# Kernel optimization log

Measured on AMD Instinct MI355X. Metric: run time of the kernel, lower is better.

## Reference

```python
import jax, jax.numpy as jnp
import numpy as np

B, S, D, K = 8, 2048, 512, 64

def setup_inputs() -> dict:
    key = jax.random.key(0)
    k1, k2, k3 = jax.random.split(key, 3)
    # glorot_uniform for weights, zeros for biases (matching Keras build)
    lim = float(np.sqrt(6.0 / (D + K)))
    return {
        "inputs": jax.random.normal(k1, (B, S, D), dtype=jnp.float32),
        "key_extract": jax.random.uniform(k2, (D, K), dtype=jnp.float32, minval=-lim, maxval=lim),
        "key_bias": jnp.zeros((1, K), dtype=jnp.float32),
        "query_extract": jax.random.uniform(k3, (D, K), dtype=jnp.float32, minval=-lim, maxval=lim),
        "query_bias": jnp.zeros((1, K), dtype=jnp.float32),
    }

def reference(inputs, key_extract, key_bias, query_extract, query_bias):
    # keys/query: [B, S, K]
    keys = jnp.einsum("bsd,dk->bsk", inputs, key_extract) + key_bias
    query = jnp.einsum("bsd,dk->bsk", inputs, query_extract) + query_bias
    # logits: [B, S, S] = query @ keys^T (no 1/sqrt(K) scaling in original)
    logits = jnp.einsum("bqk,bsk->bqs", query, keys)
    # NON-STANDARD: softmax over axis=1 (the query axis), not the last axis
    attn = jax.nn.softmax(logits, axis=1)
    # weighted_input: [B, S, D], raw inputs used as V
    return jnp.einsum("bqs,bsd->bqd", attn, inputs)
```

## Files before the change

### kernel.cpp

```cpp
#include <hip/hip_runtime.h>
#include <hip/hip_bf16.h>

#define Bn 8
#define Sn 2048
#define Dn 512
#define Kn 64

typedef _Float16 half8 __attribute__((ext_vector_type(8)));
typedef _Float16 half4v __attribute__((ext_vector_type(4)));
typedef float f32x4 __attribute__((ext_vector_type(4)));

#define MFMA16(a,b,c) __builtin_amdgcn_mfma_f32_16x16x32_f16(a,b,c,0,0,0)
#define LOG2E 1.4426950408889634f

__device__ __forceinline__ half8 ldfrag(const _Float16* base, int row, int k8){
    const int scol = k8 ^ (row & 7);
    return *(const half8*)((const char*)base + row*128 + scol*16);
}


__global__ __launch_bounds__(256) void wtrans_kernel(
    const float* __restrict__ Wk, const float* __restrict__ Wq,
    _Float16* __restrict__ Wt16)
{
    const int n = blockIdx.x;
    const int t = threadIdx.x;
    const float* src = (n < 64) ? Wq : Wk;
    const int nn = n & 63;
    #pragma unroll
    for (int i = 0; i < 2; ++i){
        const int k = t + 256*i;
        Wt16[(size_t)n*Dn + k] = (_Float16)src[(size_t)k*Kn + nn];
    }
}

__global__ __launch_bounds__(256, 2) void prep_kernel(
    const float* __restrict__ X, const _Float16* __restrict__ Wt16,
    const float* __restrict__ bk, const float* __restrict__ bq,
    _Float16* __restrict__ Qh2, _Float16* __restrict__ Kh2,
    _Float16* __restrict__ Vt2)
{
    __shared__ _Float16 Xt[2][32*64];
    const int bid = blockIdx.x;
    const int b = bid & 7, sb32 = bid >> 3;
    const int tid = threadIdx.x, lane = tid & 63, w = tid >> 6;
    const int l15 = lane & 15, l4 = lane >> 4;

    const int srow = tid >> 3, sg = tid & 7;
    const float* Xs = X + ((size_t)(b*Sn + sb32*32) + srow)*Dn + sg*8;
    const int sdst = srow*128 + (((sg ^ (srow & 7) ^ (srow >> 3)) & 7) * 16);

    const int n0 = w*32 + l15;
    const _Float16* Wp0 = Wt16 + (size_t)n0*Dn + l4*8;
    const _Float16* Wp1 = Wp0 + (size_t)16*Dn;

    f32x4 acc[2][2];
    #pragma unroll
    for (int i = 0; i < 2; ++i)
        #pragma unroll
        for (int j = 0; j < 2; ++j){ f32x4 z = {0.f,0.f,0.f,0.f}; acc[i][j] = z; }

    {
        const float4 v0 = *(const float4*)(Xs);
        const float4 v1 = *(const float4*)(Xs + 4);
        half8 h;
        h[0]=(_Float16)v0.x; h[1]=(_Float16)v0.y; h[2]=(_Float16)v0.z; h[3]=(_Float16)v0.w;
        h[4]=(_Float16)v1.x; h[5]=(_Float16)v1.y; h[6]=(_Float16)v1.z; h[7]=(_Float16)v1.w;
        *(half8*)((char*)Xt[0] + sdst) = h;
    }
    __syncthreads();

    const int dcol = w*16 + l15;
    #pragma unroll
    for (int kc = 0; kc < 8; ++kc){
        const _Float16* XtC = Xt[kc & 1];
        float4 nv0, nv1;
        if (kc < 7){
            nv0 = *(const float4*)(Xs + (kc+1)*64);
            nv1 = *(const float4*)(Xs + (kc+1)*64 + 4);
        }
        const half8 wf00 = *(const half8*)(Wp0 + kc*64);
        const half8 wf01 = *(const half8*)(Wp0 + kc*64 + 32);
        const half8 wf10 = *(const half8*)(Wp1 + kc*64);
        const half8 wf11 = *(const half8*)(Wp1 + kc*64 + 32);
        #pragma unroll
        for (int ks = 0; ks < 2; ++ks){
            #pragma unroll
            for (int qt = 0; qt < 2; ++qt){
                const int rw = qt*16 + l15;
                const int g = ((ks*4 + l4) ^ (rw & 7) ^ (rw >> 3)) & 7;
                const half8 a = *(const half8*)((const char*)XtC + rw*128 + g*16);
                acc[qt][0] = MFMA16(a, ks ? wf01 : wf00, acc[qt][0]);
                acc[qt][1] = MFMA16(a, ks ? wf11 : wf10, acc[qt][1]);
            }
        }
        {
            half8 hv;
            #pragma unroll
            for (int e = 0; e < 8; ++e){
                const int rw = l4*8 + e;
                const int g = ((dcol >> 3) ^ e ^ l4) & 7;
                hv[e] = XtC[rw*64 + g*8 + (dcol & 7)];
            }
            const size_t G = (((size_t)(b*32 + (sb32 >> 1))*2 + (sb32 & 1))*32 + kc*4 + w)*64 + lane;
            *(half8*)(Vt2 + G*8) = hv;
        }
        if (kc < 7){
            half8 h;
            h[0]=(_Float16)nv0.x; h[1]=(_Float16)nv0.y; h[2]=(_Float16)nv0.z; h[3]=(_Float16)nv0.w;
            h[4]=(_Float16)nv1.x; h[5]=(_Float16)nv1.y; h[6]=(_Float16)nv1.z; h[7]=(_Float16)nv1.w;
            *(half8*)((char*)Xt[(kc+1) & 1] + sdst) = h;
        }
        __syncthreads();
    }

    _Float16* tile16 = &Xt[0][0];
    #pragma unroll
    for (int qt = 0; qt < 2; ++qt){
        const int ql = qt*16 + l4*4;
        #pragma unroll
        for (int nt = 0; nt < 2; ++nt){
            const int n = w*32 + nt*16 + l15;
            const bool isQ = (n < 64);
            const float bias = isQ ? bq[n] : bk[n - 64];
            const float scale = isQ ? LOG2E : 1.0f;
            #pragma unroll
            for (int r = 0; r < 4; ++r)
                tile16[(ql + r)*128 + n] = (_Float16)((acc[qt][nt][r] + bias) * scale);
        }
    }
    __syncthreads();
    #pragma unroll
    for (int i = 0; i < 2; ++i){
        const int g = tid + 256*i;
        const int isK = g >> 8, qtl = (g >> 7) & 1, ks = (g >> 6) & 1, ln = g & 63;
        const int l4g = ln >> 4, l15g = ln & 15;
        const half8 h = *(const half8*)&tile16[(qtl*16 + l15g)*128 + isK*64 + ks*32 + l4g*8];
        const size_t tg = (size_t)b*128 + sb32*2 + qtl;
        _Float16* dst = (isK ? Kh2 : Qh2) + ((tg*2 + ks)*64 + ln)*8;
        *(half8*)dst = h;
    }
}

#define SBODY(QC0,QC1,QC2,QC3, QN0,QN1,QN2,QN3) do { \
    QN0 = *(const half8*)(Qp); \
    QN1 = *(const half8*)(Qp + 1024); \
    QN2 = *(const half8*)(Qp + 2048); \
    QN3 = *(const half8*)(Qp + 3072); \
    Qp += 8192; \
    f32x4 c0 = cinit, c1 = cinit; \
    c0 = MFMA16(ka0, QC0, c0); c0 = MFMA16(ka1, QC1, c0); \
    c1 = MFMA16(ka0, QC2, c1); c1 = MFMA16(ka1, QC3, c1); \
    _Pragma("unroll") \
    for (int r = 0; r < 4; ++r) \
        z[r] += exp2f(c0[r]) + exp2f(c1[r]); \
} while(0)

__global__ __launch_bounds__(512, 2) void stats_kernel(
    const _Float16* __restrict__ Qh2, const _Float16* __restrict__ Kh2,
    float* __restrict__ CS)
{
    __shared__ float zred[2][64];
    const int bid = blockIdx.x;
    const int b = bid & 7, stb = bid >> 3;
    const int tid = threadIdx.x, lane = tid & 63, w = tid >> 6;
    const int l15 = lane & 15, l4 = lane >> 4;
    const int sw = w & 3, qh = w >> 2, qh2 = qh*2;

    const half8 ka0 = *(const half8*)(Kh2 + ((size_t)((b*128 + stb*4 + sw)*2 + 0)*64 + lane)*8);
    const half8 ka1 = *(const half8*)(Kh2 + ((size_t)((b*128 + stb*4 + sw)*2 + 1)*64 + lane)*8);

    const char* Qp = (const char*)Qh2 + (size_t)(b*128 + qh2)*2048 + lane*16;

    const f32x4 cinit = {-64.f, -64.f, -64.f, -64.f};
    float z[4] = {0.f, 0.f, 0.f, 0.f};

    half8 qbA0, qbA1, qbA2, qbA3, qbB0, qbB1, qbB2, qbB3;
    qbA0 = *(const half8*)(Qp);
    qbA1 = *(const half8*)(Qp + 1024);
    qbA2 = *(const half8*)(Qp + 2048);
    qbA3 = *(const half8*)(Qp + 3072);
    Qp += 8192;

    for (int qc = 0; qc < 32; qc += 2){
        SBODY(qbA0,qbA1,qbA2,qbA3, qbB0,qbB1,qbB2,qbB3);
        SBODY(qbB0,qbB1,qbB2,qbB3, qbA0,qbA1,qbA2,qbA3);
    }
    #pragma unroll
    for (int d = 1; d < 16; d <<= 1)
        #pragma unroll
        for (int r = 0; r < 4; ++r)
            z[r] += __shfl_xor(z[r], d);
    if (l15 == 0){
        const int sl = sw*16 + l4*4;
        #pragma unroll
        for (int r = 0; r < 4; ++r) zred[qh][sl+r] = z[r];
    }
    __syncthreads();
    if (tid < 64)
        CS[b*Sn + stb*64 + tid] = -(64.0f + __log2f(zred[0][tid] + zred[1][tid]));
}

#define WRP(PT, QT, C) do { \
    half4v p; \
    p[0] = (_Float16)exp2f(C[0]); \
    p[1] = (_Float16)exp2f(C[1]); \
    p[2] = (_Float16)exp2f(C[2]); \
    p[3] = (_Float16)exp2f(C[3]); \
    const int q_ = (QT)*16 + l15; \
    *(half4v*)((char*)(PT) + q_*128 + (sb2 ^ ((q_ & 7) << 4))) = p; \
} while(0)

#define ABODY(KA, KAN, VB, VBN, CSV, CSN, PT) do { \
    f32x4 c0 = {CSV.x, CSV.y, CSV.z, CSV.w}; \
    f32x4 c1 = c0, c2 = c0, c3 = c0; \
    c0 = MFMA16(KA[0], qb[0][0], c0); c0 = MFMA16(KA[1], qb[0][1], c0); \
    c1 = MFMA16(KA[0], qb[1][0], c1); c1 = MFMA16(KA[1], qb[1][1], c1); \
    c2 = MFMA16(KA[0], qb[2][0], c2); c2 = MFMA16(KA[1], qb[2][1], c2); \
    c3 = MFMA16(KA[0], qb[3][0], c3); c3 = MFMA16(KA[1], qb[3][1], c3); \
    KAN[0] = *(const half8*)(Kp); \
    KAN[1] = *(const half8*)(Kp + 1024); \
    Kp += 8192; \
    WRP(PT, 0, c0); WRP(PT, 1, c1); \
    WRP(PT, 2, c2); WRP(PT, 3, c3); \
    asm volatile("s_waitcnt lgkmcnt(0)\n\ts_barrier" ::: "memory"); \
    CSN = *(const float4*)Cp; Cp += 64; \
    _Pragma("unroll") \
    for (int d_ = 0; d_ < 4; ++d_){ \
        VBN[d_]   = *(const half8*)(Vp0 + d_*1024); \
        VBN[4+d_] = *(const half8*)(Vp1 + d_*1024); \
    } \
    Vp0 += 65536; Vp1 += 65536; \
    __builtin_amdgcn_s_setprio(1); \
    _Pragma("unroll") \
    for (int ks = 0; ks < 2; ++ks){ \
        const half8 pa0 = ldfrag(PT, 0*16 + l15, ks*4 + l4); \
        const half8 pa1 = ldfrag(PT, 1*16 + l15, ks*4 + l4); \
        const half8 pa2 = ldfrag(PT, 2*16 + l15, ks*4 + l4); \
        const half8 pa3 = ldfrag(PT, 3*16 + l15, ks*4 + l4); \
        _Pragma("unroll") \
        for (int d_ = 0; d_ < 4; ++d_){ \
            acc[0][d_] = MFMA16(pa0, VB[ks*4+d_], acc[0][d_]); \
            acc[1][d_] = MFMA16(pa1, VB[ks*4+d_], acc[1][d_]); \
            acc[2][d_] = MFMA16(pa2, VB[ks*4+d_], acc[2][d_]); \
            acc[3][d_] = MFMA16(pa3, VB[ks*4+d_], acc[3][d_]); \
        } \
    } \
    __builtin_amdgcn_s_setprio(0); \
} while(0)

__global__ __launch_bounds__(256, 2) void attn_kernel(
    const _Float16* __restrict__ Qh2, const _Float16* __restrict__ Kh2,
    const _Float16* __restrict__ Vt2, const float* __restrict__ CS,
    float* __restrict__ out)
{
    __shared__ _Float16 Pt[2][64*64];
    const int bid = blockIdx.x;
    const int b  = bid & 7;
    const int qi = (bid >> 3) & 31;
    const int dh = bid >> 8;
    const int q0 = qi * 64;
    const int tid = threadIdx.x, lane = tid & 63, w = tid >> 6;
    const int l15 = lane & 15, l4 = lane >> 4;
    const int soff = w*16 + l4*4;
    const int sb2  = soff * 2;

    const size_t qgb = (size_t)b*128 + qi*4;
    half8 qb[4][2];
    #pragma unroll
    for (int qt = 0; qt < 4; ++qt)
        #pragma unroll
        for (int ks = 0; ks < 2; ++ks)
            qb[qt][ks] = *(const half8*)(Qh2 + (((qgb + qt)*2 + ks)*64 + lane)*8);

    const char* Kp  = (const char*)Kh2 + (size_t)(b*128 + w)*2048 + lane*16;
    const char* Vp0 = (const char*)Vt2 + (size_t)(b*2048 + dh*16 + w*4)*1024 + lane*16;
    const char* Vp1 = Vp0 + 32768;
    const float* Cp = CS + b*Sn + soff;

    half8 kaA[2], kaB[2], vbA[8], vbB[8];
    float4 csA, csB;
    kaA[0] = *(const half8*)(Kp);
    kaA[1] = *(const half8*)(Kp + 1024);
    Kp += 8192;
    #pragma unroll
    for (int d_ = 0; d_ < 4; ++d_){
        vbA[d_]   = *(const half8*)(Vp0 + d_*1024);
        vbA[4+d_] = *(const half8*)(Vp1 + d_*1024);
    }
    Vp0 += 65536; Vp1 += 65536;
    csA = *(const float4*)Cp; Cp += 64;

    f32x4 acc[4][4];
    #pragma unroll
    for (int i = 0; i < 4; ++i)
        #pragma unroll
        for (int j = 0; j < 4; ++j){ f32x4 zz4 = {0.f,0.f,0.f,0.f}; acc[i][j] = zz4; }

    for (int it = 0; it < 16; ++it){
        ABODY(kaA, kaB, vbA, vbB, csA, csB, Pt[0]);
        ABODY(kaB, kaA, vbB, vbA, csB, csA, Pt[1]);
    }

    float* ob = out + (size_t)(b*Sn + q0)*Dn + dh*256 + w*64;
    #pragma unroll
    for (int qt = 0; qt < 4; ++qt){
        const int q = qt*16 + l4*4;
        #pragma unroll
        for (int d_ = 0; d_ < 4; ++d_){
            #pragma unroll
            for (int r = 0; r < 4; ++r)
                ob[(size_t)(q + r)*Dn + d_*16 + l15] = acc[qt][d_][r];
        }
    }
}

extern "C" void kernel_launch(void* const* d_in, const int* in_sizes, int n_in,
                              void* d_out, int out_size, void* d_ws, size_t ws_size,
                              hipStream_t stream)
{
    const float* X  = (const float*)d_in[0];
    const float* Wk = (const float*)d_in[1];
    const float* bk = (const float*)d_in[2];
    const float* Wq = (const float*)d_in[3];
    const float* bq = (const float*)d_in[4];
    float* out = (float*)d_out;

    char* ws = (char*)d_ws;
    _Float16* Qh2  = (_Float16*)ws;
    _Float16* Kh2  = (_Float16*)(ws + ((size_t)2 << 20));
    _Float16* Vt2  = (_Float16*)(ws + ((size_t)4 << 20));
    float*    CS   = (float*)(ws + ((size_t)20 << 20));
    _Float16* Wt16 = (_Float16*)(ws + ((size_t)20 << 20) + (2 << 16));

    wtrans_kernel<<<dim3(128), dim3(256), 0, stream>>>(Wk, Wq, Wt16);
    prep_kernel<<<dim3(Bn*(Sn/32)), dim3(256), 0, stream>>>(X, Wt16, bk, bq, Qh2, Kh2, Vt2);
    stats_kernel<<<dim3(Bn*(Sn/64)), dim3(512), 0, stream>>>(Qh2, Kh2, CS);
    attn_kernel<<<dim3(Bn*(Sn/64)*2), dim3(256), 0, stream>>>(Qh2, Kh2, Vt2, CS, out);
}
```

Before: 82.29 us.

## Double query tile per block and stage V tiles in LDS via direct global-to-LDS loads

The attention kernel now uses 512-thread blocks covering 128 queries instead of 64, halving the grid. Each V tile is loaded once per block into shared memory with global_load_lds and double-buffered, so eight waves share it rather than each wave holding V in registers. Shared-memory offsets are precomputed, and an extra barrier per step protects the buffers. This cuts global V traffic and register pressure, but adds LDS reads, barrier synchronisation and a larger shared-memory footprint that may lower occupancy.

```diff
diff --git a/kernel.cpp b/kernel.cpp
--- a/kernel.cpp
+++ b/kernel.cpp
@@ -12,6 +12,12 @@
 
 #define MFMA16(a,b,c) __builtin_amdgcn_mfma_f32_16x16x32_f16(a,b,c,0,0,0)
 #define LOG2E 1.4426950408889634f
+
+__device__ __forceinline__ void glds16(const void* g, void* l){
+    __builtin_amdgcn_global_load_lds(
+        (const __attribute__((address_space(1))) unsigned int*)g,
+        (__attribute__((address_space(3))) unsigned int*)l, 16, 0, 0);
+}
 
 __device__ __forceinline__ half8 ldfrag(const _Float16* base, int row, int k8){
     const int scol = k8 ^ (row & 7);
@@ -201,18 +207,21 @@
         CS[b*Sn + stb*64 + tid] = -(64.0f + __log2f(zred[0][tid] + zred[1][tid]));
 }
 
-#define WRP(PT, QT, C) do { \
+#define WRP(CUR, QT, C) do { \
     half4v p; \
     p[0] = (_Float16)exp2f(C[0]); \
     p[1] = (_Float16)exp2f(C[1]); \
     p[2] = (_Float16)exp2f(C[2]); \
     p[3] = (_Float16)exp2f(C[3]); \
-    const int q_ = (QT)*16 + l15; \
-    *(half4v*)((char*)(PT) + q_*128 + (sb2 ^ ((q_ & 7) << 4))) = p; \
+    *(half4v*)((char*)Pt[CUR] + pwo[QT]) = p; \
 } while(0)
 
-#define ABODY(KA, KAN, VB, VBN, CSV, CSN, PT) do { \
-    f32x4 c0 = {CSV.x, CSV.y, CSV.z, CSV.w}; \
+#define ABODY(CUR, KA, KAN, CSA, CSN, SCV) do { \
+    { const size_t sb_ = Vbase + (size_t)((SCV)+1)*65536; \
+      _Pragma("unroll") \
+      for (int j = 0; j < 4; ++j) \
+        glds16(Vt2c + sb_ + soff[j], (char*)VL[(CUR)^1] + (w*4+j)*1024); } \
+    f32x4 c0 = {CSA.x, CSA.y, CSA.z, CSA.w}; \
     f32x4 c1 = c0, c2 = c0, c3 = c0; \
     c0 = MFMA16(KA[0], qb[0][0], c0); c0 = MFMA16(KA[1], qb[0][1], c0); \
     c1 = MFMA16(KA[0], qb[1][0], c1); c1 = MFMA16(KA[1], qb[1][1], c1); \
@@ -221,51 +230,46 @@
     KAN[0] = *(const half8*)(Kp); \
     KAN[1] = *(const half8*)(Kp + 1024); \
     Kp += 8192; \
-    WRP(PT, 0, c0); WRP(PT, 1, c1); \
-    WRP(PT, 2, c2); WRP(PT, 3, c3); \
-    asm volatile("s_waitcnt lgkmcnt(0)\n\ts_barrier" ::: "memory"); \
     CSN = *(const float4*)Cp; Cp += 64; \
-    _Pragma("unroll") \
-    for (int d_ = 0; d_ < 4; ++d_){ \
-        VBN[d_]   = *(const half8*)(Vp0 + d_*1024); \
-        VBN[4+d_] = *(const half8*)(Vp1 + d_*1024); \
-    } \
-    Vp0 += 65536; Vp1 += 65536; \
-    __builtin_amdgcn_s_setprio(1); \
-    _Pragma("unroll") \
-    for (int ks = 0; ks < 2; ++ks){ \
-        const half8 pa0 = ldfrag(PT, 0*16 + l15, ks*4 + l4); \
-        const half8 pa1 = ldfrag(PT, 1*16 + l15, ks*4 + l4); \
-        const half8 pa2 = ldfrag(PT, 2*16 + l15, ks*4 + l4); \
-        const half8 pa3 = ldfrag(PT, 3*16 + l15, ks*4 + l4); \
+    WRP(CUR, 0, c0); WRP(CUR, 1, c1); WRP(CUR, 2, c2); WRP(CUR, 3, c3); \
+    asm volatile("s_waitcnt lgkmcnt(0) vmcnt(4)\n\ts_barrier" ::: "memory"); \
+    { const char* PB = (const char*)Pt[CUR]; \
+      const char* VB_ = (const char*)VL[CUR]; \
+      _Pragma("unroll") \
+      for (int ks = 0; ks < 2; ++ks){ \
+        const half8 pa0 = *(const half8*)(PB + pao[0][ks]); \
+        const half8 pa1 = *(const half8*)(PB + pao[1][ks]); \
+        const half8 pa2 = *(const half8*)(PB + pao[2][ks]); \
+        const half8 pa3 = *(const half8*)(PB + pao[3][ks]); \
         _Pragma("unroll") \
-        for (int d_ = 0; d_ < 4; ++d_){ \
-            acc[0][d_] = MFMA16(pa0, VB[ks*4+d_], acc[0][d_]); \
-            acc[1][d_] = MFMA16(pa1, VB[ks*4+d_], acc[1][d_]); \
-            acc[2][d_] = MFMA16(pa2, VB[ks*4+d_], acc[2][d_]); \
-            acc[3][d_] = MFMA16(pa3, VB[ks*4+d_], acc[3][d_]); \
+        for (int dt = 0; dt < 4; ++dt){ \
+            const half8 vb = *(const half8*)(VB_ + vbo[ks][dt]); \
+            acc[0][dt] = MFMA16(pa0, vb, acc[0][dt]); \
+            acc[1][dt] = MFMA16(pa1, vb, acc[1][dt]); \
+            acc[2][dt] = MFMA16(pa2, vb, acc[2][dt]); \
+            acc[3][dt] = MFMA16(pa3, vb, acc[3][dt]); \
         } \
-    } \
-    __builtin_amdgcn_s_setprio(0); \
+      } } \
+    asm volatile("s_barrier" ::: "memory"); \
 } while(0)
 
-__global__ __launch_bounds__(256, 2) void attn_kernel(
+__global__ __launch_bounds__(512, 2) void attn_kernel(
     const _Float16* __restrict__ Qh2, const _Float16* __restrict__ Kh2,
     const _Float16* __restrict__ Vt2, const float* __restrict__ CS,
     float* __restrict__ out)
 {
-    __shared__ _Float16 Pt[2][64*64];
+    __shared__ _Float16 Pt[2][128*64];
+    __shared__ _Float16 VL[2][32*512];
     const int bid = blockIdx.x;
     const int b  = bid & 7;
-    const int qi = (bid >> 3) & 31;
-    const int dh = bid >> 8;
-    const int q0 = qi * 64;
+    const int qi = (bid >> 3) & 15;
+    const int dh = bid >> 7;
+    const int q0 = qi * 128;
     const int tid = threadIdx.x, lane = tid & 63, w = tid >> 6;
     const int l15 = lane & 15, l4 = lane >> 4;
-    const int soff = w*16 + l4*4;
-    const int sb2  = soff * 2;
-
-    const size_t qgb = (size_t)b*128 + qi*4;
+    const int st = w & 3, qh = w >> 2, dw = w & 3;
+
+    const size_t qgb = (size_t)b*128 + qi*8 + qh*4;
     half8 qb[4][2];
     #pragma unroll
     for (int qt = 0; qt < 4; ++qt)
@@ -273,23 +277,44 @@
         for (int ks = 0; ks < 2; ++ks)
             qb[qt][ks] = *(const half8*)(Qh2 + (((qgb + qt)*2 + ks)*64 + lane)*8);
 
-    const char* Kp  = (const char*)Kh2 + (size_t)(b*128 + w)*2048 + lane*16;
-    const char* Vp0 = (const char*)Vt2 + (size_t)(b*2048 + dh*16 + w*4)*1024 + lane*16;
-    const char* Vp1 = Vp0 + 32768;
-    const float* Cp = CS + b*Sn + soff;
-
-    half8 kaA[2], kaB[2], vbA[8], vbB[8];
+    int pwo[4], pao[4][2], vbo[2][4];
+    {
+        const int sb2 = (st*16 + l4*4) * 2;
+        #pragma unroll
+        for (int qt = 0; qt < 4; ++qt){
+            const int q_ = qh*64 + qt*16 + l15;
+            pwo[qt] = q_*128 + (sb2 ^ ((q_ & 7) << 4));
+            #pragma unroll
+            for (int ks = 0; ks < 2; ++ks)
+                pao[qt][ks] = q_*128 + (((ks*4 + l4) ^ (q_ & 7)) * 16);
+        }
+        #pragma unroll
+        for (int ks = 0; ks < 2; ++ks)
+            #pragma unroll
+            for (int dt = 0; dt < 4; ++dt)
+                vbo[ks][dt] = (ks*16 + dw*4 + dt)*1024 + lane*16;
+    }
+    const char* Vt2c = (const char*)Vt2;
+    const size_t Vbase = (size_t)b * (32*65536);
+    size_t soff[4];
+    #pragma unroll
+    for (int j = 0; j < 4; ++j){
+        const int gi = w*4 + j;
+        soff[j] = (size_t)(((gi >> 4)*32) + dh*16 + (gi & 15))*1024 + lane*16;
+    }
+
+    const char* Kp = (const char*)Kh2 + (size_t)(b*128 + st)*2048 + lane*16;
+    const float* Cp = CS + b*Sn + st*16 + l4*4;
+
+    half8 kaA[2], kaB[2];
     float4 csA, csB;
     kaA[0] = *(const half8*)(Kp);
     kaA[1] = *(const half8*)(Kp + 1024);
     Kp += 8192;
-    #pragma unroll
-    for (int d_ = 0; d_ < 4; ++d_){
-        vbA[d_]   = *(const half8*)(Vp0 + d_*1024);
-        vbA[4+d_] = *(const half8*)(Vp1 + d_*1024);
-    }
-    Vp0 += 65536; Vp1 += 65536;
     csA = *(const float4*)Cp; Cp += 64;
+    #pragma unroll
+    for (int j = 0; j < 4; ++j)
+        glds16(Vt2c + Vbase + soff[j], (char*)VL[0] + (w*4+j)*1024);
 
     f32x4 acc[4][4];
     #pragma unroll
@@ -297,20 +322,20 @@
         #pragma unroll
         for (int j = 0; j < 4; ++j){ f32x4 zz4 = {0.f,0.f,0.f,0.f}; acc[i][j] = zz4; }
 
-    for (int it = 0; it < 16; ++it){
-        ABODY(kaA, kaB, vbA, vbB, csA, csB, Pt[0]);
-        ABODY(kaB, kaA, vbB, vbA, csB, csA, Pt[1]);
-    }
-
-    float* ob = out + (size_t)(b*Sn + q0)*Dn + dh*256 + w*64;
+    for (int sc = 0; sc < 32; sc += 2){
+        ABODY(0, kaA, kaB, csA, csB, sc);
+        ABODY(1, kaB, kaA, csB, csA, sc+1);
+    }
+
+    float* ob = out + (size_t)(b*Sn + q0 + qh*64)*Dn + dh*256 + dw*64;
     #pragma unroll
     for (int qt = 0; qt < 4; ++qt){
         const int q = qt*16 + l4*4;
         #pragma unroll
-        for (int d_ = 0; d_ < 4; ++d_){
+        for (int dt = 0; dt < 4; ++dt){
             #pragma unroll
             for (int r = 0; r < 4; ++r)
-                ob[(size_t)(q + r)*Dn + d_*16 + l15] = acc[qt][d_][r];
+                ob[(size_t)(q + r)*Dn + dt*16 + l15] = acc[qt][dt][r];
         }
     }
 }
@@ -336,5 +361,5 @@
     wtrans_kernel<<<dim3(128), dim3(256), 0, stream>>>(Wk, Wq, Wt16);
     prep_kernel<<<dim3(Bn*(Sn/32)), dim3(256), 0, stream>>>(X, Wt16, bk, bq, Qh2, Kh2, Vt2);
     stats_kernel<<<dim3(Bn*(Sn/64)), dim3(512), 0, stream>>>(Qh2, Kh2, CS);
-    attn_kernel<<<dim3(Bn*(Sn/64)*2), dim3(256), 0, stream>>>(Qh2, Kh2, Vt2, CS, out);
-}
+    attn_kernel<<<dim3(Bn*(Sn/128)*2), dim3(512), 0, stream>>>(Qh2, Kh2, Vt2, CS, out);
+}
```

Measured after the change: 89.66 us. +9.0%, slower.

## Materialize unnormalized P in global memory and fold softmax scale into V

Applied to the files above, without the earlier changes.

The stats kernel now computes per-key column max and sum, then runs a second QK^T pass that writes exp(logit - max) as fp16 P tiles to a global buffer. A new vscale kernel multiplies V by the per-key normalization factor. The attention kernel then becomes a pure P·V GEMM streaming P and V from global memory, with no recomputation of QK^T and no LDS exchange or barriers. In exchange it adds a large P write and read (B*S*S fp16, about 64 MB), an extra kernel launch, and precision risk from scaling fp16 V.

```diff
diff --git a/kernel.cpp b/kernel.cpp
--- a/kernel.cpp
+++ b/kernel.cpp
@@ -12,11 +12,6 @@
 
 #define MFMA16(a,b,c) __builtin_amdgcn_mfma_f32_16x16x32_f16(a,b,c,0,0,0)
 #define LOG2E 1.4426950408889634f
-
-__device__ __forceinline__ half8 ldfrag(const _Float16* base, int row, int k8){
-    const int scol = k8 ^ (row & 7);
-    return *(const half8*)((const char*)base + row*128 + scol*16);
-}
 
 
 __global__ __launch_bounds__(256) void wtrans_kernel(
@@ -142,175 +137,210 @@
     }
 }
 
-#define SBODY(QC0,QC1,QC2,QC3, QN0,QN1,QN2,QN3) do { \
-    QN0 = *(const half8*)(Qp); \
-    QN1 = *(const half8*)(Qp + 1024); \
-    QN2 = *(const half8*)(Qp + 2048); \
-    QN3 = *(const half8*)(Qp + 3072); \
-    Qp += 8192; \
-    f32x4 c0 = cinit, c1 = cinit; \
-    c0 = MFMA16(ka0, QC0, c0); c0 = MFMA16(ka1, QC1, c0); \
-    c1 = MFMA16(ka0, QC2, c1); c1 = MFMA16(ka1, QC3, c1); \
-    _Pragma("unroll") \
-    for (int r = 0; r < 4; ++r) \
-        z[r] += exp2f(c0[r]) + exp2f(c1[r]); \
-} while(0)
-
-__global__ __launch_bounds__(512, 2) void stats_kernel(
+__global__ __launch_bounds__(512) void stats2_kernel(
     const _Float16* __restrict__ Qh2, const _Float16* __restrict__ Kh2,
-    float* __restrict__ CS)
-{
-    __shared__ float zred[2][64];
+    _Float16* __restrict__ Pg, float* __restrict__ CSV)
+{
+    __shared__ float mred[8][64];
+    __shared__ float zred[8][64];
+    __shared__ float mfin[64];
+    __shared__ char  tr[8][2048];
     const int bid = blockIdx.x;
     const int b = bid & 7, stb = bid >> 3;
     const int tid = threadIdx.x, lane = tid & 63, w = tid >> 6;
     const int l15 = lane & 15, l4 = lane >> 4;
-    const int sw = w & 3, qh = w >> 2, qh2 = qh*2;
-
-    const half8 ka0 = *(const half8*)(Kh2 + ((size_t)((b*128 + stb*4 + sw)*2 + 0)*64 + lane)*8);
-    const half8 ka1 = *(const half8*)(Kh2 + ((size_t)((b*128 + stb*4 + sw)*2 + 1)*64 + lane)*8);
-
-    const char* Qp = (const char*)Qh2 + (size_t)(b*128 + qh2)*2048 + lane*16;
-
-    const f32x4 cinit = {-64.f, -64.f, -64.f, -64.f};
-    float z[4] = {0.f, 0.f, 0.f, 0.f};
-
-    half8 qbA0, qbA1, qbA2, qbA3, qbB0, qbB1, qbB2, qbB3;
-    qbA0 = *(const half8*)(Qp);
-    qbA1 = *(const half8*)(Qp + 1024);
-    qbA2 = *(const half8*)(Qp + 2048);
-    qbA3 = *(const half8*)(Qp + 3072);
-    Qp += 8192;
-
-    for (int qc = 0; qc < 32; qc += 2){
-        SBODY(qbA0,qbA1,qbA2,qbA3, qbB0,qbB1,qbB2,qbB3);
-        SBODY(qbB0,qbB1,qbB2,qbB3, qbA0,qbA1,qbA2,qbA3);
+
+    half8 ka[4][2];
+    #pragma unroll
+    for (int ssub = 0; ssub < 4; ++ssub)
+        #pragma unroll
+        for (int ks = 0; ks < 2; ++ks)
+            ka[ssub][ks] = *(const half8*)((const char*)Kh2 +
+                (((size_t)(b*128 + stb*4 + ssub)*2 + ks) << 10) + lane*16);
+
+    const char* Qb = (const char*)Qh2 + ((size_t)(b*128 + w*16)*2 << 10) + lane*16;
+
+    f32x4 m4[4], z4[4];
+    #pragma unroll
+    for (int s = 0; s < 4; ++s){
+        f32x4 mi = {-3.0e38f,-3.0e38f,-3.0e38f,-3.0e38f};
+        f32x4 zi = {0.f,0.f,0.f,0.f};
+        m4[s] = mi; z4[s] = zi;
+    }
+    for (int qi = 0; qi < 16; ++qi){
+        const half8 qb0 = *(const half8*)(Qb + qi*2048);
+        const half8 qb1 = *(const half8*)(Qb + qi*2048 + 1024);
+        #pragma unroll
+        for (int ssub = 0; ssub < 4; ++ssub){
+            f32x4 c = {0.f,0.f,0.f,0.f};
+            c = MFMA16(ka[ssub][0], qb0, c);
+            c = MFMA16(ka[ssub][1], qb1, c);
+            #pragma unroll
+            for (int r = 0; r < 4; ++r){
+                m4[ssub][r] = fmaxf(m4[ssub][r], c[r]);
+                z4[ssub][r] += exp2f(c[r] - 64.0f);
+            }
+        }
     }
     #pragma unroll
     for (int d = 1; d < 16; d <<= 1)
         #pragma unroll
-        for (int r = 0; r < 4; ++r)
-            z[r] += __shfl_xor(z[r], d);
+        for (int ssub = 0; ssub < 4; ++ssub)
+            #pragma unroll
+            for (int r = 0; r < 4; ++r){
+                m4[ssub][r] = fmaxf(m4[ssub][r], __shfl_xor(m4[ssub][r], d));
+                z4[ssub][r] += __shfl_xor(z4[ssub][r], d);
+            }
     if (l15 == 0){
-        const int sl = sw*16 + l4*4;
-        #pragma unroll
-        for (int r = 0; r < 4; ++r) zred[qh][sl+r] = z[r];
+        #pragma unroll
+        for (int ssub = 0; ssub < 4; ++ssub)
+            #pragma unroll
+            for (int r = 0; r < 4; ++r){
+                mred[w][ssub*16 + l4*4 + r] = m4[ssub][r];
+                zred[w][ssub*16 + l4*4 + r] = z4[ssub][r];
+            }
     }
     __syncthreads();
-    if (tid < 64)
-        CS[b*Sn + stb*64 + tid] = -(64.0f + __log2f(zred[0][tid] + zred[1][tid]));
-}
-
-#define WRP(PT, QT, C) do { \
-    half4v p; \
-    p[0] = (_Float16)exp2f(C[0]); \
-    p[1] = (_Float16)exp2f(C[1]); \
-    p[2] = (_Float16)exp2f(C[2]); \
-    p[3] = (_Float16)exp2f(C[3]); \
-    const int q_ = (QT)*16 + l15; \
-    *(half4v*)((char*)(PT) + q_*128 + (sb2 ^ ((q_ & 7) << 4))) = p; \
+    if (tid < 64){
+        float M = mred[0][tid], Z = zred[0][tid];
+        #pragma unroll
+        for (int ww = 1; ww < 8; ++ww){
+            M = fmaxf(M, mred[ww][tid]);
+            Z += zred[ww][tid];
+        }
+        mfin[tid] = M;
+        CSV[b*Sn + stb*64 + tid] = exp2f(M - 64.0f - __log2f(Z));
+    }
+    __syncthreads();
+
+    float4 Mloc[4];
+    #pragma unroll
+    for (int ssub = 0; ssub < 4; ++ssub)
+        Mloc[ssub] = *(const float4*)&mfin[ssub*16 + l4*4];
+
+    char* trw = tr[w];
+    char* PgB = (char*)Pg + (size_t)(b*32 + stb)*262144 + (size_t)(w*16)*2048 + lane*16;
+    for (int qi = 0; qi < 16; ++qi){
+        const half8 qb0 = *(const half8*)(Qb + qi*2048);
+        const half8 qb1 = *(const half8*)(Qb + qi*2048 + 1024);
+        #pragma unroll
+        for (int ssub = 0; ssub < 4; ++ssub){
+            f32x4 c = {0.f,0.f,0.f,0.f};
+            c = MFMA16(ka[ssub][0], qb0, c);
+            c = MFMA16(ka[ssub][1], qb1, c);
+            half4v pq;
+            pq[0] = (_Float16)exp2f(c[0] - Mloc[ssub].x);
+            pq[1] = (_Float16)exp2f(c[1] - Mloc[ssub].y);
+            pq[2] = (_Float16)exp2f(c[2] - Mloc[ssub].z);
+            pq[3] = (_Float16)exp2f(c[3] - Mloc[ssub].w);
+            *(half4v*)(trw + l15*128 + (((ssub*2 + (l4>>1)) ^ (l15 & 7)) << 4) + ((l4 & 1) << 3)) = pq;
+        }
+        #pragma unroll
+        for (int ks = 0; ks < 2; ++ks){
+            const half8 g = *(const half8*)(trw + l15*128 + (((ks*4 + l4) ^ (l15 & 7)) << 4));
+            *(half8*)(PgB + qi*2048 + ks*1024) = g;
+        }
+    }
+}
+
+__global__ __launch_bounds__(256) void vscale_kernel(
+    _Float16* __restrict__ Vt2, const float* __restrict__ CSV)
+{
+    const int o0 = blockIdx.x*256 + threadIdx.x;
+    #pragma unroll
+    for (int rep = 0; rep < 2; ++rep){
+        const int oo = o0 + rep*524288;
+        const int ln = oo & 63;
+        const int G  = oo >> 6;
+        const int ks = (G >> 5) & 1;
+        const int sc = (G >> 6) & 31;
+        const int b  = G >> 11;
+        const int s0 = sc*64 + ks*32 + (ln >> 4)*8;
+        const float4 c0 = *(const float4*)&CSV[b*Sn + s0];
+        const float4 c1 = *(const float4*)&CSV[b*Sn + s0 + 4];
+        half8 v = ((half8*)Vt2)[oo];
+        v[0] = (_Float16)((float)v[0] * c0.x);
+        v[1] = (_Float16)((float)v[1] * c0.y);
+        v[2] = (_Float16)((float)v[2] * c0.z);
+        v[3] = (_Float16)((float)v[3] * c0.w);
+        v[4] = (_Float16)((float)v[4] * c1.x);
+        v[5] = (_Float16)((float)v[5] * c1.y);
+        v[6] = (_Float16)((float)v[6] * c1.z);
+        v[7] = (_Float16)((float)v[7] * c1.w);
+        ((half8*)Vt2)[oo] = v;
+    }
+}
+
+#define GB(PA, PAN, VB, VBN) do { \
+    _Pragma("unroll") \
+    for (int qt = 0; qt < 4; ++qt){ \
+        PAN[qt][0] = *(const half8*)(PaP + qt*2048); \
+        PAN[qt][1] = *(const half8*)(PaP + qt*2048 + 1024); \
+    } \
+    PaP += 262144; \
+    _Pragma("unroll") \
+    for (int dt = 0; dt < 4; ++dt){ \
+        VBN[0][dt] = *(const half8*)(VbP + dt*1024); \
+        VBN[1][dt] = *(const half8*)(VbP + 32768 + dt*1024); \
+    } \
+    VbP += 65536; \
+    _Pragma("unroll") \
+    for (int qt = 0; qt < 4; ++qt) \
+        _Pragma("unroll") \
+        for (int dt = 0; dt < 4; ++dt){ \
+            acc[qt][dt] = MFMA16(PA[qt][0], VB[0][dt], acc[qt][dt]); \
+            acc[qt][dt] = MFMA16(PA[qt][1], VB[1][dt], acc[qt][dt]); \
+        } \
 } while(0)
 
-#define ABODY(KA, KAN, VB, VBN, CSV, CSN, PT) do { \
-    f32x4 c0 = {CSV.x, CSV.y, CSV.z, CSV.w}; \
-    f32x4 c1 = c0, c2 = c0, c3 = c0; \
-    c0 = MFMA16(KA[0], qb[0][0], c0); c0 = MFMA16(KA[1], qb[0][1], c0); \
-    c1 = MFMA16(KA[0], qb[1][0], c1); c1 = MFMA16(KA[1], qb[1][1], c1); \
-    c2 = MFMA16(KA[0], qb[2][0], c2); c2 = MFMA16(KA[1], qb[2][1], c2); \
-    c3 = MFMA16(KA[0], qb[3][0], c3); c3 = MFMA16(KA[1], qb[3][1], c3); \
-    KAN[0] = *(const half8*)(Kp); \
-    KAN[1] = *(const half8*)(Kp + 1024); \
-    Kp += 8192; \
-    WRP(PT, 0, c0); WRP(PT, 1, c1); \
-    WRP(PT, 2, c2); WRP(PT, 3, c3); \
-    asm volatile("s_waitcnt lgkmcnt(0)\n\ts_barrier" ::: "memory"); \
-    CSN = *(const float4*)Cp; Cp += 64; \
-    _Pragma("unroll") \
-    for (int d_ = 0; d_ < 4; ++d_){ \
-        VBN[d_]   = *(const half8*)(Vp0 + d_*1024); \
-        VBN[4+d_] = *(const half8*)(Vp1 + d_*1024); \
-    } \
-    Vp0 += 65536; Vp1 += 65536; \
-    __builtin_amdgcn_s_setprio(1); \
-    _Pragma("unroll") \
-    for (int ks = 0; ks < 2; ++ks){ \
-        const half8 pa0 = ldfrag(PT, 0*16 + l15, ks*4 + l4); \
-        const half8 pa1 = ldfrag(PT, 1*16 + l15, ks*4 + l4); \
-        const half8 pa2 = ldfrag(PT, 2*16 + l15, ks*4 + l4); \
-        const half8 pa3 = ldfrag(PT, 3*16 + l15, ks*4 + l4); \
-        _Pragma("unroll") \
-        for (int d_ = 0; d_ < 4; ++d_){ \
-            acc[0][d_] = MFMA16(pa0, VB[ks*4+d_], acc[0][d_]); \
-            acc[1][d_] = MFMA16(pa1, VB[ks*4+d_], acc[1][d_]); \
-            acc[2][d_] = MFMA16(pa2, VB[ks*4+d_], acc[2][d_]); \
-            acc[3][d_] = MFMA16(pa3, VB[ks*4+d_], acc[3][d_]); \
-        } \
-    } \
-    __builtin_amdgcn_s_setprio(0); \
-} while(0)
-
-__global__ __launch_bounds__(256, 2) void attn_kernel(
-    const _Float16* __restrict__ Qh2, const _Float16* __restrict__ Kh2,
-    const _Float16* __restrict__ Vt2, const float* __restrict__ CS,
+__global__ __launch_bounds__(256) void attn3_kernel(
+    const _Float16* __restrict__ Pg, const _Float16* __restrict__ Vt2,
     float* __restrict__ out)
 {
-    __shared__ _Float16 Pt[2][64*64];
     const int bid = blockIdx.x;
     const int b  = bid & 7;
     const int qi = (bid >> 3) & 31;
     const int dh = bid >> 8;
-    const int q0 = qi * 64;
     const int tid = threadIdx.x, lane = tid & 63, w = tid >> 6;
     const int l15 = lane & 15, l4 = lane >> 4;
-    const int soff = w*16 + l4*4;
-    const int sb2  = soff * 2;
-
-    const size_t qgb = (size_t)b*128 + qi*4;
-    half8 qb[4][2];
-    #pragma unroll
-    for (int qt = 0; qt < 4; ++qt)
-        #pragma unroll
-        for (int ks = 0; ks < 2; ++ks)
-            qb[qt][ks] = *(const half8*)(Qh2 + (((qgb + qt)*2 + ks)*64 + lane)*8);
-
-    const char* Kp  = (const char*)Kh2 + (size_t)(b*128 + w)*2048 + lane*16;
-    const char* Vp0 = (const char*)Vt2 + (size_t)(b*2048 + dh*16 + w*4)*1024 + lane*16;
-    const char* Vp1 = Vp0 + 32768;
-    const float* Cp = CS + b*Sn + soff;
-
-    half8 kaA[2], kaB[2], vbA[8], vbB[8];
-    float4 csA, csB;
-    kaA[0] = *(const half8*)(Kp);
-    kaA[1] = *(const half8*)(Kp + 1024);
-    Kp += 8192;
-    #pragma unroll
-    for (int d_ = 0; d_ < 4; ++d_){
-        vbA[d_]   = *(const half8*)(Vp0 + d_*1024);
-        vbA[4+d_] = *(const half8*)(Vp1 + d_*1024);
-    }
-    Vp0 += 65536; Vp1 += 65536;
-    csA = *(const float4*)Cp; Cp += 64;
+
+    const char* PaP = (const char*)Pg + (size_t)(b*32)*262144 + (size_t)(qi*4)*2048 + lane*16;
+    const char* VbP = (const char*)Vt2 + ((size_t)(b*2048 + dh*16 + w*4) << 10) + lane*16;
+
+    half8 paA[4][2], paB[4][2], vbA[2][4], vbB[2][4];
+    #pragma unroll
+    for (int qt = 0; qt < 4; ++qt){
+        paA[qt][0] = *(const half8*)(PaP + qt*2048);
+        paA[qt][1] = *(const half8*)(PaP + qt*2048 + 1024);
+    }
+    PaP += 262144;
+    #pragma unroll
+    for (int dt = 0; dt < 4; ++dt){
+        vbA[0][dt] = *(const half8*)(VbP + dt*1024);
+        vbA[1][dt] = *(const half8*)(VbP + 32768 + dt*1024);
+    }
+    VbP += 65536;
 
     f32x4 acc[4][4];
     #pragma unroll
     for (int i = 0; i < 4; ++i)
         #pragma unroll
-        for (int j = 0; j < 4; ++j){ f32x4 zz4 = {0.f,0.f,0.f,0.f}; acc[i][j] = zz4; }
-
-    for (int it = 0; it < 16; ++it){
-        ABODY(kaA, kaB, vbA, vbB, csA, csB, Pt[0]);
-        ABODY(kaB, kaA, vbB, vbA, csB, csA, Pt[1]);
-    }
-
-    float* ob = out + (size_t)(b*Sn + q0)*Dn + dh*256 + w*64;
+        for (int j = 0; j < 4; ++j){ f32x4 z = {0.f,0.f,0.f,0.f}; acc[i][j] = z; }
+
+    for (int sc = 0; sc < 16; ++sc){
+        GB(paA, paB, vbA, vbB);
+        GB(paB, paA, vbB, vbA);
+    }
+
+    float* ob = out + (size_t)(b*Sn + qi*64)*Dn + dh*256 + w*64;
     #pragma unroll
     for (int qt = 0; qt < 4; ++qt){
         const int q = qt*16 + l4*4;
         #pragma unroll
-        for (int d_ = 0; d_ < 4; ++d_){
+        for (int dt = 0; dt < 4; ++dt){
             #pragma unroll
             for (int r = 0; r < 4; ++r)
-                ob[(size_t)(q + r)*Dn + d_*16 + l15] = acc[qt][d_][r];
+                ob[(size_t)(q + r)*Dn + dt*16 + l15] = acc[qt][dt][r];
         }
     }
 }
@@ -330,11 +360,13 @@
     _Float16* Qh2  = (_Float16*)ws;
     _Float16* Kh2  = (_Float16*)(ws + ((size_t)2 << 20));
     _Float16* Vt2  = (_Float16*)(ws + ((size_t)4 << 20));
-    float*    CS   = (float*)(ws + ((size_t)20 << 20));
-    _Float16* Wt16 = (_Float16*)(ws + ((size_t)20 << 20) + (2 << 16));
+    _Float16* Wt16 = (_Float16*)(ws + ((size_t)20 << 20));
+    float*    CSV  = (float*)(ws + ((size_t)20 << 20) + (1 << 18));
+    _Float16* Pg   = (_Float16*)(ws + ((size_t)21 << 20));
 
     wtrans_kernel<<<dim3(128), dim3(256), 0, stream>>>(Wk, Wq, Wt16);
     prep_kernel<<<dim3(Bn*(Sn/32)), dim3(256), 0, stream>>>(X, Wt16, bk, bq, Qh2, Kh2, Vt2);
-    stats_kernel<<<dim3(Bn*(Sn/64)), dim3(512), 0, stream>>>(Qh2, Kh2, CS);
-    attn_kernel<<<dim3(Bn*(Sn/64)*2), dim3(256), 0, stream>>>(Qh2, Kh2, Vt2, CS, out);
-}
+    stats2_kernel<<<dim3(Bn*(Sn/64)), dim3(512), 0, stream>>>(Qh2, Kh2, Pg, CSV);
+    vscale_kernel<<<dim3(2048), dim3(256), 0, stream>>>(Vt2, CSV);
+    attn3_kernel<<<dim3(Bn*(Sn/64)*2), dim3(256), 0, stream>>>(Pg, Vt2, out);
+}
```

Result: slower. 106.2 us (+29.1%).
